# Optimization experiments

Hardware: AMD Instinct MI355X
Metric: run time of the kernel (lower is better)

The kernel has to match this reference:

```python
import jax, jax.numpy as jnp
import numpy as np

B, N = 2048, 64
D, H = 64, 256
CARD_V, UNIT_V, ENEMY_V, AT_V, SRC_V, MODE_V, TER_V, SITE_V, SKILL_V = 400, 100, 120, 50, 30, 10, 12, 25, 60
STATE_SC, CE_SC, SITE_SC, ME_SC, ACT_SC = 64, 8, 6, 8, 16
L_HAND, L_UNIT, L_CE, L_SK, L_VS, L_ME, L_TGT = 16, 8, 8, 8, 16, 16, 8
STATE_IN = STATE_SC + 6 * D + (D + CE_SC) + (D + SITE_SC) + (D + ME_SC)  # 662
ACT_IN = 7 * D + ACT_SC  # 464


def setup_inputs() -> dict:
    key = jax.random.key(0)
    ks = iter(jax.random.split(key, 64))
    nrm = lambda shape, s=1.0: jax.random.normal(next(ks), shape, jnp.float32) * s
    ri = lambda shape, hi: jax.random.randint(next(ks), shape, 0, hi, jnp.int32)
    return {
        'state_scalars': nrm((B, STATE_SC)),
        'mode_id': ri((B,), MODE_V), 'terrain_id': ri((B,), TER_V), 'site_type_id': ri((B,), SITE_V),
        'hand_ids': ri((B, L_HAND), CARD_V), 'hand_mask': ri((B, L_HAND), 2),
        'unit_ids': ri((B, L_UNIT), UNIT_V), 'unit_mask': ri((B, L_UNIT), 2),
        'combat_enemy_ids': ri((B, L_CE), ENEMY_V), 'combat_enemy_scalars': nrm((B, L_CE, CE_SC)), 'combat_enemy_mask': ri((B, L_CE), 2),
        'skill_ids': ri((B, L_SK), SKILL_V), 'skill_mask': ri((B, L_SK), 2),
        'visible_site_ids': ri((B, L_VS), SITE_V), 'visible_site_scalars': nrm((B, L_VS, SITE_SC)), 'visible_site_mask': ri((B, L_VS), 2),
        'map_enemy_ids': ri((B, L_ME), ENEMY_V), 'map_enemy_scalars': nrm((B, L_ME, ME_SC)), 'map_enemy_mask': ri((B, L_ME), 2),
        'action_ids': ri((B, N, 6), SRC_V),  # SRC_V=30 is min over the 6 id vocabs -> always in range
        'action_scalars': nrm((B, N, ACT_SC)),
        'target_enemy_ids': ri((B, N, L_TGT), ENEMY_V), 'target_mask': ri((B, N, L_TGT), 2),
        'card_emb': nrm((CARD_V, D), 0.05), 'unit_emb': nrm((UNIT_V, D), 0.05), 'enemy_emb': nrm((ENEMY_V, D), 0.05),
        'action_type_emb': nrm((AT_V, D), 0.05), 'source_emb': nrm((SRC_V, D), 0.05), 'mode_emb': nrm((MODE_V, D), 0.05),
        'terrain_emb': nrm((TER_V, D), 0.05), 'site_emb': nrm((SITE_V, D), 0.05), 'skill_emb': nrm((SKILL_V, D), 0.05),
        'map_site_emb': nrm((SITE_V, D), 0.05),
        'W_s': nrm((STATE_IN, H), 0.02), 'b_s': jnp.zeros((H,), jnp.float32),
        'W_a': nrm((ACT_IN, H), 0.02), 'b_a': jnp.zeros((H,), jnp.float32),
        'W1': nrm((2 * H, H), 0.02), 'b1': jnp.zeros((H,), jnp.float32),
        'W2': nrm((H, 1), 0.02), 'b2': jnp.zeros((1,), jnp.float32),
        'W_v': nrm((H, 1), 0.02), 'b_v': jnp.zeros((1,), jnp.float32),
    }


def masked_mean(x, mask):
    # x: [..., L, D'], mask: [..., L] (0/1). Empty list -> zeros (count clamped to 1).
    m = mask.astype(x.dtype)[..., None]
    s = jnp.sum(x * m, axis=-2)
    c = jnp.maximum(jnp.sum(m, axis=-2), 1.0)
    return s / c


def reference(state_scalars, mode_id, terrain_id, site_type_id, hand_ids, hand_mask,
              unit_ids, unit_mask, combat_enemy_ids, combat_enemy_scalars, combat_enemy_mask,
              skill_ids, skill_mask, visible_site_ids, visible_site_scalars, visible_site_mask,
              map_enemy_ids, map_enemy_scalars, map_enemy_mask, action_ids, action_scalars,
              target_enemy_ids, target_mask, card_emb, unit_emb, enemy_emb, action_type_emb,
              source_emb, mode_emb, terrain_emb, site_emb, skill_emb, map_site_emb,
              W_s, b_s, W_a, b_a, W1, b1, W2, b2, W_v, b_v):
    # ---- state encoding (batched version of encode_state) ----
    hand_pool = masked_mean(card_emb[hand_ids], hand_mask)            # [B, D]
    unit_pool = masked_mean(unit_emb[unit_ids], unit_mask)            # [B, D]
    ce = jnp.concatenate([enemy_emb[combat_enemy_ids], combat_enemy_scalars], axis=-1)
    ce_pool = masked_mean(ce, combat_enemy_mask)                      # [B, D+CE_SC]
    skill_pool = masked_mean(skill_emb[skill_ids], skill_mask)        # [B, D]
    vs = jnp.concatenate([map_site_emb[visible_site_ids], visible_site_scalars], axis=-1)
    vs_pool = masked_mean(vs, visible_site_mask)                      # [B, D+SITE_SC]
    me = jnp.concatenate([enemy_emb[map_enemy_ids], map_enemy_scalars], axis=-1)
    me_pool = masked_mean(me, map_enemy_mask)                         # [B, D+ME_SC]
    state_input = jnp.concatenate([
        state_scalars, mode_emb[mode_id], hand_pool, unit_pool,
        terrain_emb[terrain_id], site_emb[site_type_id],
        ce_pool, skill_pool, vs_pool, me_pool], axis=-1)              # [B, 662]
    state_repr = jnp.tanh(state_input @ W_s + b_s)                    # [B, H]
    # ---- action encoding (batched encode_actions) ----
    tgt_pool = masked_mean(enemy_emb[target_enemy_ids], target_mask)  # [B, N, D]
    action_input = jnp.concatenate([
        action_type_emb[action_ids[..., 0]], source_emb[action_ids[..., 1]],
        card_emb[action_ids[..., 2]], unit_emb[action_ids[..., 3]],
        enemy_emb[action_ids[..., 4]], skill_emb[action_ids[..., 5]],
        tgt_pool, action_scalars], axis=-1)                           # [B, N, 464]
    action_reprs = jnp.tanh(action_input @ W_a + b_a)                 # [B, N, H]
    # ---- scoring + value heads ----
    state_b = jnp.broadcast_to(state_repr[:, None, :], (state_repr.shape[0], action_reprs.shape[1], state_repr.shape[1]))
    combined = jnp.concatenate([state_b, action_reprs], axis=-1)      # [B, N, 2H]
    logits = (jnp.tanh(combined @ W1 + b1) @ W2 + b2)[..., 0]         # [B, N]
    value = (state_repr @ W_v + b_v)[..., 0]                          # [B]
    return logits, value
```

## Files before the change

kernel.cpp:

```cpp
#include <hip/hip_runtime.h>
#include <hip/hip_bf16.h>

#define BB 2048
#define NN 64
#define DD 64
#define HH 256
#define L_HAND 16
#define L_UNIT 8
#define L_CE 8
#define L_SK 8
#define L_VS 16
#define L_ME 16
#define L_TGT 8
#define STATE_SC 64
#define CE_SC 8
#define SITE_SC 6
#define ME_SC 8
#define ACT_SC 16
#define STATE_IN 662
#define ACT_IN 464

#define SROWS 4
#define SK 672
#define SSTRIDE 676

typedef __attribute__((ext_vector_type(8))) short short8;
typedef __attribute__((ext_vector_type(4))) float f32x4;

__device__ __forceinline__ float fast_tanh(float x) {
    float e = __expf(2.0f * x);
    return 1.0f - 2.0f / (e + 1.0f);
}
__device__ __forceinline__ short f2bs(float x) {
    __hip_bfloat16 h = __float2bfloat16(x);
    return *reinterpret_cast<short*>(&h);
}
__device__ __forceinline__ float bs2f(short u) {
    union { unsigned int i; float f; } v;
    v.i = ((unsigned int)(unsigned short)u) << 16;
    return v.f;
}

#define RO_AT    0
#define RO_SRC   50
#define RO_CARD  80
#define RO_UNIT  480
#define RO_ENEMY 580
#define RO_SKILL 700
#define EMB_ROWS 760

#define T0 (480 * 256)
#define T1 (T0 + 256 * 256)
#define T2 (T1 + EMB_ROWS * 64)
#define T3 (T2 + SK * 256)
#define T4 (T3 + 256 * 256)

__global__ __launch_bounds__(256) void pack_kernel(
    const float* __restrict__ W_a, const float* __restrict__ W1,
    const float* __restrict__ W_s,
    const float* __restrict__ at_emb, const float* __restrict__ src_emb,
    const float* __restrict__ card_emb, const float* __restrict__ unit_emb,
    const float* __restrict__ enemy_emb, const float* __restrict__ skill_emb,
    ushort* __restrict__ WaP, ushort* __restrict__ W1bP, ushort* __restrict__ emb16,
    ushort* __restrict__ WsP, ushort* __restrict__ W1aP)
{
    const int idx = blockIdx.x * 256 + threadIdx.x;
    if (idx < T0) {
        const int k = idx >> 8, n = idx & 255;
        const float v = (k < ACT_IN) ? W_a[k * HH + n] : 0.f;
        const int pi = (((k >> 5) * 16 + (n >> 4)) * 64 +
                        ((n & 15) + 16 * ((k >> 3) & 3))) * 8 + (k & 7);
        WaP[pi] = (ushort)f2bs(v);
    } else if (idx < T1) {
        const int j = idx - T0;
        const int k = j >> 8, n = j & 255;
        const float v = W1[(256 + k) * HH + n];
        const int pi = (((k >> 5) * 16 + (n >> 4)) * 64 +
                        ((n & 15) + 16 * ((k >> 3) & 3))) * 8 + (k & 7);
        W1bP[pi] = (ushort)f2bs(v);
    } else if (idx < T2) {
        const int j = idx - T1;
        const int row = j >> 6, d = j & 63;
        float v;
        if      (row < RO_SRC)   v = at_emb[row * 64 + d];
        else if (row < RO_CARD)  v = src_emb[(row - RO_SRC) * 64 + d];
        else if (row < RO_UNIT)  v = card_emb[(row - RO_CARD) * 64 + d];
        else if (row < RO_ENEMY) v = unit_emb[(row - RO_UNIT) * 64 + d];
        else if (row < RO_SKILL) v = enemy_emb[(row - RO_ENEMY) * 64 + d];
        else                     v = skill_emb[(row - RO_SKILL) * 64 + d];
        emb16[j] = (ushort)f2bs(v);
    } else if (idx < T3) {
        const int j = idx - T2;
        const int k = j >> 8, n = j & 255;
        const float v = (k < STATE_IN) ? W_s[k * HH + n] : 0.f;
        const int pi = (((k >> 5) * 16 + (n >> 4)) * 64 +
                        ((n & 15) + 16 * ((k >> 3) & 3))) * 8 + (k & 7);
        WsP[pi] = (ushort)f2bs(v);
    } else if (idx < T4) {
        const int j = idx - T3;
        const int k = j >> 8, n = j & 255;
        const float v = W1[k * HH + n];
        const int pi = (((k >> 5) * 16 + (n >> 4)) * 64 +
                        ((n & 15) + 16 * ((k >> 3) & 3))) * 8 + (k & 7);
        W1aP[pi] = (ushort)f2bs(v);
    }
}

__global__ __launch_bounds__(256) void state_mfma_kernel(
    const float* __restrict__ state_scalars,
    const int* __restrict__ mode_id, const int* __restrict__ terrain_id,
    const int* __restrict__ site_type_id,
    const int* __restrict__ hand_ids, const int* __restrict__ hand_mask,
    const int* __restrict__ unit_ids, const int* __restrict__ unit_mask,
    const int* __restrict__ ce_ids, const float* __restrict__ ce_sc, const int* __restrict__ ce_mask,
    const int* __restrict__ skill_ids, const int* __restrict__ skill_mask,
    const int* __restrict__ vs_ids, const float* __restrict__ vs_sc, const int* __restrict__ vs_mask,
    const int* __restrict__ me_ids, const float* __restrict__ me_sc, const int* __restrict__ me_mask,
    const float* __restrict__ card_emb, const float* __restrict__ unit_emb,
    const float* __restrict__ enemy_emb, const float* __restrict__ mode_emb,
    const float* __restrict__ ter_emb, const float* __restrict__ site_emb,
    const float* __restrict__ skill_emb, const float* __restrict__ msite_emb,
    const ushort* __restrict__ WsP, const float* __restrict__ b_s,
    const ushort* __restrict__ W1aP,
    const float* __restrict__ W_v, const float* __restrict__ b_v,
    float* __restrict__ s_part, float* __restrict__ out_value)
{
    __shared__ float s_in[SROWS * SSTRIDE];
    __shared__ ushort sA2[8 * 64 * 8];
    __shared__ float red[4][4];

    const int t = threadIdx.x;
    const int b0 = blockIdx.x * SROWS;
    const int w = t >> 6;
    const int lane = t & 63;

    for (int r = 0; r < SROWS; ++r) {
        const int b = b0 + r;
        for (int o = t; o < SK; o += 256) {
            float v;
            if (o >= STATE_IN) {
                v = 0.f;
            } else if (o < 64) {
                v = state_scalars[b * STATE_SC + o];
            } else if (o < 128) {
                v = mode_emb[mode_id[b] * DD + (o - 64)];
            } else if (o < 192) {
                const int d = o - 128; float s = 0.f; int c = 0;
                for (int l = 0; l < L_HAND; ++l) {
                    const int m = hand_mask[b * L_HAND + l]; c += m;
                    if (m) s += card_emb[hand_ids[b * L_HAND + l] * DD + d];
                }
                v = s / (float)(c > 1 ? c : 1);
            } else if (o < 256) {
                const int d = o - 192; float s = 0.f; int c = 0;
                for (int l = 0; l < L_UNIT; ++l) {
                    const int m = unit_mask[b * L_UNIT + l]; c += m;
                    if (m) s += unit_emb[unit_ids[b * L_UNIT + l] * DD + d];
                }
                v = s / (float)(c > 1 ? c : 1);
            } else if (o < 320) {
                v = ter_emb[terrain_id[b] * DD + (o - 256)];
            } else if (o < 384) {
                v = site_emb[site_type_id[b] * DD + (o - 320)];
            } else if (o < 456) {
                const int d = o - 384; float s = 0.f; int c = 0;
                for (int l = 0; l < L_CE; ++l) {
                    const int m = ce_mask[b * L_CE + l]; c += m;
                    if (m) s += (d < 64) ? enemy_emb[ce_ids[b * L_CE + l] * DD + d]
                                         : ce_sc[(b * L_CE + l) * CE_SC + (d - 64)];
                }
                v = s / (float)(c > 1 ? c : 1);
            } else if (o < 520) {
                const int d = o - 456; float s = 0.f; int c = 0;
                for (int l = 0; l < L_SK; ++l) {
                    const int m = skill_mask[b * L_SK + l]; c += m;
                    if (m) s += skill_emb[skill_ids[b * L_SK + l] * DD + d];
                }
                v = s / (float)(c > 1 ? c : 1);
            } else if (o < 590) {
                const int d = o - 520; float s = 0.f; int c = 0;
                for (int l = 0; l < L_VS; ++l) {
                    const int m = vs_mask[b * L_VS + l]; c += m;
                    if (m) s += (d < 64) ? msite_emb[vs_ids[b * L_VS + l] * DD + d]
                                         : vs_sc[(b * L_VS + l) * SITE_SC + (d - 64)];
                }
                v = s / (float)(c > 1 ? c : 1);
            } else {
                const int d = o - 590; float s = 0.f; int c = 0;
                for (int l = 0; l < L_ME; ++l) {
                    const int m = me_mask[b * L_ME + l]; c += m;
                    if (m) s += (d < 64) ? enemy_emb[me_ids[b * L_ME + l] * DD + d]
                                         : me_sc[(b * L_ME + l) * ME_SC + (d - 64)];
                }
                v = s / (float)(c > 1 ? c : 1);
            }
            s_in[r * SSTRIDE + o] = v;
        }
    }
    __syncthreads();

    const short8* Ws8  = (const short8*)WsP;
    const short8* W1a8 = (const short8*)W1aP;
    const f32x4 zero = {0.f, 0.f, 0.f, 0.f};
    const int m15 = lane & 15;
    const int g = lane >> 4;
    const float* arow = s_in + (m15 & 3) * SSTRIDE;

    f32x4 acc1[4];
#pragma unroll
    for (int nt = 0; nt < 4; ++nt) acc1[nt] = zero;

    for (int kt = 0; kt < 21; ++kt) {
        const int k0 = kt * 32 + 8 * g;
        const float4 v0 = *(const float4*)(arow + k0);
        const float4 v1 = *(const float4*)(arow + k0 + 4);
        short8 a;
        a[0] = f2bs(v0.x); a[1] = f2bs(v0.y); a[2] = f2bs(v0.z); a[3] = f2bs(v0.w);
        a[4] = f2bs(v1.x); a[5] = f2bs(v1.y); a[6] = f2bs(v1.z); a[7] = f2bs(v1.w);
        short8 bfr[4];
#pragma unroll
        for (int nt = 0; nt < 4; ++nt) bfr[nt] = Ws8[(kt * 16 + w * 4 + nt) * 64 + lane];
#pragma unroll
        for (int nt = 0; nt < 4; ++nt)
            acc1[nt] = __builtin_amdgcn_mfma_f32_16x16x32_bf16(a, bfr[nt], acc1[nt], 0, 0, 0);
    }

    float sr[4][4];
    float pv[4] = {0.f, 0.f, 0.f, 0.f};
#pragma unroll
    for (int nt = 0; nt < 4; ++nt) {
        const int n = w * 64 + nt * 16 + m15;
        const float bsn = b_s[n];
        const float wvn = W_v[n];
#pragma unroll
        for (int r = 0; r < 4; ++r) {
            const float sv = fast_tanh(acc1[nt][r] + bsn);
            sr[nt][r] = sv;
            pv[r] = fmaf(sv, wvn, pv[r]);
        }
    }
#pragma unroll
    for (int r = 0; r < 4; ++r) {
        float v = pv[r];
        v += __shfl_xor(v, 1);
        v += __shfl_xor(v, 2);
        v += __shfl_xor(v, 4);
        v += __shfl_xor(v, 8);
        if (lane == 0) red[w][r] = v;
    }
    if (g == 0) {
#pragma unroll
        for (int nt = 0; nt < 4; ++nt) {
            const int n = w * 64 + nt * 16 + m15;
            const int kt2 = n >> 5;
            const int lo16 = (n >> 3) & 3;
#pragma unroll
            for (int r = 0; r < 4; ++r) {
                const int pi = (kt2 * 64 + (r + 16 * lo16)) * 8 + (n & 7);
                sA2[pi] = (ushort)f2bs(sr[nt][r]);
            }
        }
    }
    __syncthreads();

    if (t < SROWS) {
        out_value[b0 + t] = red[0][t] + red[1][t] + red[2][t] + red[3][t] + b_v[0];
    }

    const short8* sA2_8 = (const short8*)sA2;
    f32x4 acc2[4];
#pragma unroll
    for (int nt = 0; nt < 4; ++nt) acc2[nt] = zero;
#pragma unroll
    for (int kt = 0; kt < 8; ++kt) {
        const short8 a2 = sA2_8[kt * 64 + lane];
        short8 bfr[4];
#pragma unroll
        for (int nt = 0; nt < 4; ++nt) bfr[nt] = W1a8[(kt * 16 + w * 4 + nt) * 64 + lane];
#pragma unroll
        for (int nt = 0; nt < 4; ++nt)
            acc2[nt] = __builtin_amdgcn_mfma_f32_16x16x32_bf16(a2, bfr[nt], acc2[nt], 0, 0, 0);
    }
    if (g == 0) {
#pragma unroll
        for (int nt = 0; nt < 4; ++nt) {
            const int n = w * 64 + nt * 16 + m15;
#pragma unroll
            for (int r = 0; r < 4; ++r)
                s_part[(b0 + r) * HH + n] = acc2[nt][r];
        }
    }
}

__global__ __launch_bounds__(512) void action_mfma_kernel(
    const int* __restrict__ action_ids, const float* __restrict__ action_scalars,
    const int* __restrict__ tgt_ids, const int* __restrict__ tgt_mask,
    const ushort* __restrict__ emb16,
    const ushort* __restrict__ WaP, const float* __restrict__ b_a,
    const ushort* __restrict__ W1bP, const float* __restrict__ b1,
    const float* __restrict__ W2, const float* __restrict__ b2,
    const float* __restrict__ s_part, float* __restrict__ out_logits)
{
    __shared__ ushort sA[15 * 4 * 64 * 8];
    __shared__ float red[8][64];
    __shared__ int s_ids[64 * 6];
    __shared__ int s_tid[64 * 8];
    __shared__ int s_tmk[64 * 8];

    const int t = threadIdx.x;
    const int b = blockIdx.x;
    const int w = t >> 6;
    const int lane = t & 63;

    for (int i = t; i < 64 * 6; i += 512) s_ids[i] = action_ids[b * (64 * 6) + i];
    for (int i = t; i < 64 * 8; i += 512) {
        s_tid[i] = tgt_ids[b * (64 * 8) + i];
        s_tmk[i] = tgt_mask[b * (64 * 8) + i];
    }
    __syncthreads();

    {
        const int m = lane;
        const int mt = m >> 4;
        const int mrow = m & 15;
        const ushort* enemy16 = emb16 + RO_ENEMY * 64;
        short8* sA8w = (short8*)sA;
        for (int kc = w; kc < 60; kc += 8) {
            const int k0 = kc << 3;
            short8 val;
            if (k0 < 384) {
                const int j = k0 >> 6;
                int roff;
                if      (j == 0) roff = RO_AT;
                else if (j == 1) roff = RO_SRC;
                else if (j == 2) roff = RO_CARD;
                else if (j == 3) roff = RO_UNIT;
                else if (j == 4) roff = RO_ENEMY;
                else             roff = RO_SKILL;
                const int id = s_ids[m * 6 + j];
                val = *(const short8*)(emb16 + (roff + id) * 64 + (k0 & 63));
            } else if (k0 < 448) {
                const int d = k0 - 384;
                float accq[8] = {0.f, 0.f, 0.f, 0.f, 0.f, 0.f, 0.f, 0.f};
                int c = 0;
#pragma unroll
                for (int l = 0; l < L_TGT; ++l) {
                    const int mk = s_tmk[m * 8 + l];
                    c += mk;
                    const float fm = (float)mk;
                    const short8 e = *(const short8*)(enemy16 + s_tid[m * 8 + l] * 64 + d);
#pragma unroll
                    for (int q = 0; q < 8; ++q) accq[q] = fmaf(fm, bs2f(e[q]), accq[q]);
                }
                const float inv = 1.0f / (float)(c > 1 ? c : 1);
#pragma unroll
                for (int q = 0; q < 8; ++q) val[q] = f2bs(accq[q] * inv);
            } else if (k0 < 464) {
                const float* sc = action_scalars + (b * NN + m) * ACT_SC + (k0 - 448);
                const float4 f0 = *(const float4*)sc;
                const float4 f1 = *(const float4*)(sc + 4);
                val[0] = f2bs(f0.x); val[1] = f2bs(f0.y); val[2] = f2bs(f0.z); val[3] = f2bs(f0.w);
                val[4] = f2bs(f1.x); val[5] = f2bs(f1.y); val[6] = f2bs(f1.z); val[7] = f2bs(f1.w);
            } else {
#pragma unroll
                for (int q = 0; q < 8; ++q) val[q] = 0;
            }
            const int kt = k0 >> 5, lo = (k0 >> 3) & 3;
            sA8w[(kt * 4 + mt) * 64 + mrow + 16 * lo] = val;
        }
    }
    __syncthreads();

    const short8* sA8  = (const short8*)sA;
    const short8* Wa8  = (const short8*)WaP;
    const short8* W1b8 = (const short8*)W1bP;
    const f32x4 zero = {0.f, 0.f, 0.f, 0.f};
    const int m15 = lane & 15;

    float ba[2];
#pragma unroll
    for (int nt = 0; nt < 2; ++nt) ba[nt] = b_a[w * 32 + nt * 16 + m15];

    f32x4 acc[4][2];
#pragma unroll
    for (int i = 0; i < 4; ++i) { acc[i][0] = zero; acc[i][1] = zero; }

    short8 bn0 = Wa8[(w * 2 + 0) * 64 + lane];
    short8 bn1 = Wa8[(w * 2 + 1) * 64 + lane];
#pragma unroll
    for (int kt = 0; kt < 15; ++kt) {
        const short8 b0 = bn0, b1 = bn1;
        if (kt < 14) {
            bn0 = Wa8[((kt + 1) * 16 + w * 2 + 0) * 64 + lane];
            bn1 = Wa8[((kt + 1) * 16 + w * 2 + 1) * 64 + lane];
        }
        short8 a[4];
#pragma unroll
        for (int mti = 0; mti < 4; ++mti) a[mti] = sA8[(kt * 4 + mti) * 64 + lane];
#pragma unroll
        for (int mti = 0; mti < 4; ++mti) {
            acc[mti][0] = __builtin_amdgcn_mfma_f32_16x16x32_bf16(a[mti], b0, acc[mti][0], 0, 0, 0);
            acc[mti][1] = __builtin_amdgcn_mfma_f32_16x16x32_bf16(a[mti], b1, acc[mti][1], 0, 0, 0);
        }
    }

    __syncthreads();

    short8 cn0 = W1b8[(w * 2 + 0) * 64 + lane];
    short8 cn1 = W1b8[(w * 2 + 1) * 64 + lane];

#pragma unroll
    for (int mti = 0; mti < 4; ++mti)
#pragma unroll
        for (int nt = 0; nt < 2; ++nt) {
            const int n = w * 32 + nt * 16 + m15;
            const int kt2 = n >> 5;
            const int lo16 = (n >> 3) & 3;
#pragma unroll
            for (int r = 0; r < 4; ++r) {
                const int mm = mti * 16 + (lane >> 4) * 4 + r;
                const float h = fast_tanh(acc[mti][nt][r] + ba[nt]);
                const int pi = ((kt2 * 4 + mti) * 64 + ((mm & 15) + 16 * lo16)) * 8 + (n & 7);
                sA[pi] = (ushort)f2bs(h);
            }
        }
    __syncthreads();

    float sp[2], w2v[2];
#pragma unroll
    for (int nt = 0; nt < 2; ++nt) {
        const int n = w * 32 + nt * 16 + m15;
        sp[nt]  = s_part[b * HH + n] + b1[n];
        w2v[nt] = W2[n];
    }

#pragma unroll
    for (int i = 0; i < 4; ++i) { acc[i][0] = zero; acc[i][1] = zero; }

#pragma unroll
    for (int kt = 0; kt < 8; ++kt) {
        const short8 b0 = cn0, b1 = cn1;
        if (kt < 7) {
            cn0 = W1b8[((kt + 1) * 16 + w * 2 + 0) * 64 + lane];
            cn1 = W1b8[((kt + 1) * 16 + w * 2 + 1) * 64 + lane];
        }
        short8 a[4];
#pragma unroll
        for (int mti = 0; mti < 4; ++mti) a[mti] = sA8[(kt * 4 + mti) * 64 + lane];
#pragma unroll
        for (int mti = 0; mti < 4; ++mti) {
            acc[mti][0] = __builtin_amdgcn_mfma_f32_16x16x32_bf16(a[mti], b0, acc[mti][0], 0, 0, 0);
            acc[mti][1] = __builtin_amdgcn_mfma_f32_16x16x32_bf16(a[mti], b1, acc[mti][1], 0, 0, 0);
        }
    }

    float part[4][4];
#pragma unroll
    for (int mti = 0; mti < 4; ++mti)
#pragma unroll
        for (int r = 0; r < 4; ++r) part[mti][r] = 0.f;

#pragma unroll
    for (int mti = 0; mti < 4; ++mti)
#pragma unroll
        for (int nt = 0; nt < 2; ++nt)
#pragma unroll
            for (int r = 0; r < 4; ++r)
                part[mti][r] += fast_tanh(acc[mti][nt][r] + sp[nt]) * w2v[nt];

#pragma unroll
    for (int mti = 0; mti < 4; ++mti)
#pragma unroll
        for (int r = 0; r < 4; ++r) {
            float v = part[mti][r];
            v += __shfl_xor(v, 1);
            v += __shfl_xor(v, 2);
            v += __shfl_xor(v, 4);
            v += __shfl_xor(v, 8);
            part[mti][r] = v;
        }
    if (m15 == 0) {
#pragma unroll
        for (int mti = 0; mti < 4; ++mti)
#pragma unroll
            for (int r = 0; r < 4; ++r) {
                const int mm = mti * 16 + (lane >> 4) * 4 + r;
                red[w][mm] = part[mti][r];
            }
    }
    __syncthreads();
    if (t < 64) {
        float s = b2[0];
#pragma unroll
        for (int wi = 0; wi < 8; ++wi) s += red[wi][t];
        out_logits[b * NN + t] = s;
    }
}

extern "C" void kernel_launch(void* const* d_in, const int* in_sizes, int n_in,
                              void* d_out, int out_size, void* d_ws, size_t ws_size,
                              hipStream_t stream) {
    const float* state_scalars = (const float*)d_in[0];
    const int*   mode_id       = (const int*)d_in[1];
    const int*   terrain_id    = (const int*)d_in[2];
    const int*   site_type_id  = (const int*)d_in[3];
    const int*   hand_ids      = (const int*)d_in[4];
    const int*   hand_mask     = (const int*)d_in[5];
    const int*   unit_ids      = (const int*)d_in[6];
    const int*   unit_mask     = (const int*)d_in[7];
    const int*   ce_ids        = (const int*)d_in[8];
    const float* ce_sc         = (const float*)d_in[9];
    const int*   ce_mask       = (const int*)d_in[10];
    const int*   skill_ids     = (const int*)d_in[11];
    const int*   skill_mask    = (const int*)d_in[12];
    const int*   vs_ids        = (const int*)d_in[13];
    const float* vs_sc         = (const float*)d_in[14];
    const int*   vs_mask       = (const int*)d_in[15];
    const int*   me_ids        = (const int*)d_in[16];
    const float* me_sc         = (const float*)d_in[17];
    const int*   me_mask       = (const int*)d_in[18];
    const int*   action_ids    = (const int*)d_in[19];
    const float* action_scalars= (const float*)d_in[20];
    const int*   tgt_ids       = (const int*)d_in[21];
    const int*   tgt_mask      = (const int*)d_in[22];
    const float* card_emb      = (const float*)d_in[23];
    const float* unit_emb      = (const float*)d_in[24];
    const float* enemy_emb     = (const float*)d_in[25];
    const float* at_emb        = (const float*)d_in[26];
    const float* src_emb       = (const float*)d_in[27];
    const float* mode_emb      = (const float*)d_in[28];
    const float* ter_emb       = (const float*)d_in[29];
    const float* site_emb      = (const float*)d_in[30];
    const float* skill_emb     = (const float*)d_in[31];
    const float* msite_emb     = (const float*)d_in[32];
    const float* W_s           = (const float*)d_in[33];
    const float* b_s           = (const float*)d_in[34];
    const float* W_a           = (const float*)d_in[35];
    const float* b_a           = (const float*)d_in[36];
    const float* W1            = (const float*)d_in[37];
    const float* b1            = (const float*)d_in[38];
    const float* W2            = (const float*)d_in[39];
    const float* b2            = (const float*)d_in[40];
    const float* W_v           = (const float*)d_in[41];
    const float* b_v           = (const float*)d_in[42];

    float* out_logits = (float*)d_out;
    float* out_value  = (float*)d_out + (size_t)BB * NN;

    char* ws = (char*)d_ws;
    float*  s_part = (float*)ws;
    ushort* WaP    = (ushort*)(ws + 2097152);
    ushort* W1bP   = (ushort*)(ws + 2342912);
    ushort* emb16  = (ushort*)(ws + 2473984);
    ushort* WsP    = (ushort*)(ws + 2571264);
    ushort* W1aP   = (ushort*)(ws + 2915328);

    pack_kernel<<<(T4 + 255) / 256, 256, 0, stream>>>(
        W_a, W1, W_s, at_emb, src_emb, card_emb, unit_emb, enemy_emb, skill_emb,
        WaP, W1bP, emb16, WsP, W1aP);

    state_mfma_kernel<<<BB / SROWS, 256, 0, stream>>>(
        state_scalars, mode_id, terrain_id, site_type_id,
        hand_ids, hand_mask, unit_ids, unit_mask,
        ce_ids, ce_sc, ce_mask, skill_ids, skill_mask,
        vs_ids, vs_sc, vs_mask, me_ids, me_sc, me_mask,
        card_emb, unit_emb, enemy_emb, mode_emb, ter_emb, site_emb,
        skill_emb, msite_emb,
        WsP, b_s, W1aP, W_v, b_v, s_part, out_value);

    action_mfma_kernel<<<BB, 512, 0, stream>>>(
        action_ids, action_scalars, tgt_ids, tgt_mask,
        emb16, WaP, b_a, W1bP, b1, W2, b2, s_part, out_logits);
}
```

Measured before the change: 132.5 us.

## Vectorize state gathers with bf16 tables and split action A-tile into halves

The state kernel's per-element gather loop becomes per-thread 8-wide chunk work. It uses vector loads and the bf16 packed embedding tables for card, unit, enemy and skill, and uses branchless masked FMAs in place of scalar fp32 reads. The action kernel builds its A operand in two halves. The shared buffer shrinks from 15 to 8 k-tiles, and the second half is rebuilt after the first half's MFMAs. This cuts LDS use, which may raise occupancy, but it adds two barriers and serializes the gather with compute. Reading bf16 embeddings in the state path also slightly changes numerics.

```diff
diff --git a/kernel.cpp b/kernel.cpp
--- a/kernel.cpp
+++ b/kernel.cpp
@@ -116,10 +116,9 @@
     const int* __restrict__ skill_ids, const int* __restrict__ skill_mask,
     const int* __restrict__ vs_ids, const float* __restrict__ vs_sc, const int* __restrict__ vs_mask,
     const int* __restrict__ me_ids, const float* __restrict__ me_sc, const int* __restrict__ me_mask,
-    const float* __restrict__ card_emb, const float* __restrict__ unit_emb,
-    const float* __restrict__ enemy_emb, const float* __restrict__ mode_emb,
-    const float* __restrict__ ter_emb, const float* __restrict__ site_emb,
-    const float* __restrict__ skill_emb, const float* __restrict__ msite_emb,
+    const float* __restrict__ mode_emb, const float* __restrict__ ter_emb,
+    const float* __restrict__ site_emb, const float* __restrict__ msite_emb,
+    const ushort* __restrict__ emb16,
     const ushort* __restrict__ WsP, const float* __restrict__ b_s,
     const ushort* __restrict__ W1aP,
     const float* __restrict__ W_v, const float* __restrict__ b_v,
@@ -133,68 +132,171 @@
     const int b0 = blockIdx.x * SROWS;
     const int w = t >> 6;
     const int lane = t & 63;
-
-    for (int r = 0; r < SROWS; ++r) {
-        const int b = b0 + r;
-        for (int o = t; o < SK; o += 256) {
-            float v;
-            if (o >= STATE_IN) {
-                v = 0.f;
-            } else if (o < 64) {
-                v = state_scalars[b * STATE_SC + o];
-            } else if (o < 128) {
-                v = mode_emb[mode_id[b] * DD + (o - 64)];
-            } else if (o < 192) {
-                const int d = o - 128; float s = 0.f; int c = 0;
-                for (int l = 0; l < L_HAND; ++l) {
-                    const int m = hand_mask[b * L_HAND + l]; c += m;
-                    if (m) s += card_emb[hand_ids[b * L_HAND + l] * DD + d];
-                }
-                v = s / (float)(c > 1 ? c : 1);
-            } else if (o < 256) {
-                const int d = o - 192; float s = 0.f; int c = 0;
-                for (int l = 0; l < L_UNIT; ++l) {
-                    const int m = unit_mask[b * L_UNIT + l]; c += m;
-                    if (m) s += unit_emb[unit_ids[b * L_UNIT + l] * DD + d];
-                }
-                v = s / (float)(c > 1 ? c : 1);
-            } else if (o < 320) {
-                v = ter_emb[terrain_id[b] * DD + (o - 256)];
-            } else if (o < 384) {
-                v = site_emb[site_type_id[b] * DD + (o - 320)];
-            } else if (o < 456) {
-                const int d = o - 384; float s = 0.f; int c = 0;
-                for (int l = 0; l < L_CE; ++l) {
-                    const int m = ce_mask[b * L_CE + l]; c += m;
-                    if (m) s += (d < 64) ? enemy_emb[ce_ids[b * L_CE + l] * DD + d]
-                                         : ce_sc[(b * L_CE + l) * CE_SC + (d - 64)];
-                }
-                v = s / (float)(c > 1 ? c : 1);
-            } else if (o < 520) {
-                const int d = o - 456; float s = 0.f; int c = 0;
-                for (int l = 0; l < L_SK; ++l) {
-                    const int m = skill_mask[b * L_SK + l]; c += m;
-                    if (m) s += skill_emb[skill_ids[b * L_SK + l] * DD + d];
-                }
-                v = s / (float)(c > 1 ? c : 1);
-            } else if (o < 590) {
-                const int d = o - 520; float s = 0.f; int c = 0;
-                for (int l = 0; l < L_VS; ++l) {
-                    const int m = vs_mask[b * L_VS + l]; c += m;
-                    if (m) s += (d < 64) ? msite_emb[vs_ids[b * L_VS + l] * DD + d]
-                                         : vs_sc[(b * L_VS + l) * SITE_SC + (d - 64)];
-                }
-                v = s / (float)(c > 1 ? c : 1);
-            } else {
-                const int d = o - 590; float s = 0.f; int c = 0;
-                for (int l = 0; l < L_ME; ++l) {
-                    const int m = me_mask[b * L_ME + l]; c += m;
-                    if (m) s += (d < 64) ? enemy_emb[me_ids[b * L_ME + l] * DD + d]
-                                         : me_sc[(b * L_ME + l) * ME_SC + (d - 64)];
-                }
-                v = s / (float)(c > 1 ? c : 1);
-            }
-            s_in[r * SSTRIDE + o] = v;
+    const ushort* card16  = emb16 + RO_CARD  * 64;
+    const ushort* unit16  = emb16 + RO_UNIT  * 64;
+    const ushort* enemy16 = emb16 + RO_ENEMY * 64;
+    const ushort* skill16 = emb16 + RO_SKILL * 64;
+
+    for (int u = t; u < SROWS * 84; u += 256) {
+        const int r  = u / 84;
+        const int un = u - r * 84;
+        const int b  = b0 + r;
+        float* dst = s_in + r * SSTRIDE;
+        if (un < 8) {
+            const int o0 = un * 8;
+            const float4 f0 = *(const float4*)(state_scalars + b * STATE_SC + o0);
+            const float4 f1 = *(const float4*)(state_scalars + b * STATE_SC + o0 + 4);
+            *(float4*)(dst + o0) = f0; *(float4*)(dst + o0 + 4) = f1;
+        } else if (un < 16) {
+            const int d0 = (un - 8) * 8;
+            const float4 f0 = *(const float4*)(mode_emb + mode_id[b] * DD + d0);
+            const float4 f1 = *(const float4*)(mode_emb + mode_id[b] * DD + d0 + 4);
+            *(float4*)(dst + 64 + d0) = f0; *(float4*)(dst + 64 + d0 + 4) = f1;
+        } else if (un < 24) {
+            const int d0 = (un - 16) * 8;
+            float acc[8] = {0,0,0,0,0,0,0,0}; int c = 0;
+#pragma unroll
+            for (int l = 0; l < L_HAND; ++l) {
+                const int mk = hand_mask[b * L_HAND + l]; c += mk;
+                const float fm = (float)mk;
+                const short8 e = *(const short8*)(card16 + hand_ids[b * L_HAND + l] * 64 + d0);
+#pragma unroll
+                for (int q = 0; q < 8; ++q) acc[q] = fmaf(fm, bs2f(e[q]), acc[q]);
+            }
+            const float inv = 1.0f / (float)(c > 1 ? c : 1);
+#pragma unroll
+            for (int q = 0; q < 8; ++q) dst[128 + d0 + q] = acc[q] * inv;
+        } else if (un < 32) {
+            const int d0 = (un - 24) * 8;
+            float acc[8] = {0,0,0,0,0,0,0,0}; int c = 0;
+#pragma unroll
+            for (int l = 0; l < L_UNIT; ++l) {
+                const int mk = unit_mask[b * L_UNIT + l]; c += mk;
+                const float fm = (float)mk;
+                const short8 e = *(const short8*)(unit16 + unit_ids[b * L_UNIT + l] * 64 + d0);
+#pragma unroll
+                for (int q = 0; q < 8; ++q) acc[q] = fmaf(fm, bs2f(e[q]), acc[q]);
+            }
+            const float inv = 1.0f / (float)(c > 1 ? c : 1);
+#pragma unroll
+            for (int q = 0; q < 8; ++q) dst[192 + d0 + q] = acc[q] * inv;
+        } else if (un < 40) {
+            const int d0 = (un - 32) * 8;
+            const float4 f0 = *(const float4*)(ter_emb + terrain_id[b] * DD + d0);
+            const float4 f1 = *(const float4*)(ter_emb + terrain_id[b] * DD + d0 + 4);
+            *(float4*)(dst + 256 + d0) = f0; *(float4*)(dst + 256 + d0 + 4) = f1;
+        } else if (un < 48) {
+            const int d0 = (un - 40) * 8;
+            const float4 f0 = *(const float4*)(site_emb + site_type_id[b] * DD + d0);
+            const float4 f1 = *(const float4*)(site_emb + site_type_id[b] * DD + d0 + 4);
+            *(float4*)(dst + 320 + d0) = f0; *(float4*)(dst + 320 + d0 + 4) = f1;
+        } else if (un < 56) {
+            const int d0 = (un - 48) * 8;
+            float acc[8] = {0,0,0,0,0,0,0,0}; int c = 0;
+#pragma unroll
+            for (int l = 0; l < L_CE; ++l) {
+                const int mk = ce_mask[b * L_CE + l]; c += mk;
+                const float fm = (float)mk;
+                const short8 e = *(const short8*)(enemy16 + ce_ids[b * L_CE + l] * 64 + d0);
+#pragma unroll
+                for (int q = 0; q < 8; ++q) acc[q] = fmaf(fm, bs2f(e[q]), acc[q]);
+            }
+            const float inv = 1.0f / (float)(c > 1 ? c : 1);
+#pragma unroll
+            for (int q = 0; q < 8; ++q) dst[384 + d0 + q] = acc[q] * inv;
+        } else if (un == 56) {
+            float acc[8] = {0,0,0,0,0,0,0,0}; int c = 0;
+#pragma unroll
+            for (int l = 0; l < L_CE; ++l) {
+                const int mk = ce_mask[b * L_CE + l]; c += mk;
+                const float fm = (float)mk;
+                const float4 f0 = *(const float4*)(ce_sc + (b * L_CE + l) * CE_SC);
+                const float4 f1 = *(const float4*)(ce_sc + (b * L_CE + l) * CE_SC + 4);
+                acc[0] = fmaf(fm, f0.x, acc[0]); acc[1] = fmaf(fm, f0.y, acc[1]);
+                acc[2] = fmaf(fm, f0.z, acc[2]); acc[3] = fmaf(fm, f0.w, acc[3]);
+                acc[4] = fmaf(fm, f1.x, acc[4]); acc[5] = fmaf(fm, f1.y, acc[5]);
+                acc[6] = fmaf(fm, f1.z, acc[6]); acc[7] = fmaf(fm, f1.w, acc[7]);
+            }
+            const float inv = 1.0f / (float)(c > 1 ? c : 1);
+#pragma unroll
+            for (int q = 0; q < 8; ++q) dst[448 + q] = acc[q] * inv;
+        } else if (un < 65) {
+            const int d0 = (un - 57) * 8;
+            float acc[8] = {0,0,0,0,0,0,0,0}; int c = 0;
+#pragma unroll
+            for (int l = 0; l < L_SK; ++l) {
+                const int mk = skill_mask[b * L_SK + l]; c += mk;
+                const float fm = (float)mk;
+                const short8 e = *(const short8*)(skill16 + skill_ids[b * L_SK + l] * 64 + d0);
+#pragma unroll
+                for (int q = 0; q < 8; ++q) acc[q] = fmaf(fm, bs2f(e[q]), acc[q]);
+            }
+            const float inv = 1.0f / (float)(c > 1 ? c : 1);
+#pragma unroll
+            for (int q = 0; q < 8; ++q) dst[456 + d0 + q] = acc[q] * inv;
+        } else if (un < 73) {
+            const int d0 = (un - 65) * 8;
+            float acc[8] = {0,0,0,0,0,0,0,0}; int c = 0;
+#pragma unroll
+            for (int l = 0; l < L_VS; ++l) {
+                const int mk = vs_mask[b * L_VS + l]; c += mk;
+                const float fm = (float)mk;
+                const float4 f0 = *(const float4*)(msite_emb + vs_ids[b * L_VS + l] * DD + d0);
+                const float4 f1 = *(const float4*)(msite_emb + vs_ids[b * L_VS + l] * DD + d0 + 4);
+                acc[0] = fmaf(fm, f0.x, acc[0]); acc[1] = fmaf(fm, f0.y, acc[1]);
+                acc[2] = fmaf(fm, f0.z, acc[2]); acc[3] = fmaf(fm, f0.w, acc[3]);
+                acc[4] = fmaf(fm, f1.x, acc[4]); acc[5] = fmaf(fm, f1.y, acc[5]);
+                acc[6] = fmaf(fm, f1.z, acc[6]); acc[7] = fmaf(fm, f1.w, acc[7]);
+            }
+            const float inv = 1.0f / (float)(c > 1 ? c : 1);
+#pragma unroll
+            for (int q = 0; q < 8; ++q) dst[520 + d0 + q] = acc[q] * inv;
+        } else if (un == 73) {
+            float acc[6] = {0,0,0,0,0,0}; int c = 0;
+#pragma unroll
+            for (int l = 0; l < L_VS; ++l) {
+                const int mk = vs_mask[b * L_VS + l]; c += mk;
+                const float fm = (float)mk;
+                const float* p = vs_sc + (b * L_VS + l) * SITE_SC;
+#pragma unroll
+                for (int q = 0; q < 6; ++q) acc[q] = fmaf(fm, p[q], acc[q]);
+            }
+            const float inv = 1.0f / (float)(c > 1 ? c : 1);
+#pragma unroll
+            for (int q = 0; q < 6; ++q) dst[584 + q] = acc[q] * inv;
+        } else if (un < 82) {
+            const int d0 = (un - 74) * 8;
+            float acc[8] = {0,0,0,0,0,0,0,0}; int c = 0;
+#pragma unroll
+            for (int l = 0; l < L_ME; ++l) {
+                const int mk = me_mask[b * L_ME + l]; c += mk;
+                const float fm = (float)mk;
+                const short8 e = *(const short8*)(enemy16 + me_ids[b * L_ME + l] * 64 + d0);
+#pragma unroll
+                for (int q = 0; q < 8; ++q) acc[q] = fmaf(fm, bs2f(e[q]), acc[q]);
+            }
+            const float inv = 1.0f / (float)(c > 1 ? c : 1);
+#pragma unroll
+            for (int q = 0; q < 8; ++q) dst[590 + d0 + q] = acc[q] * inv;
+        } else if (un == 82) {
+            float acc[8] = {0,0,0,0,0,0,0,0}; int c = 0;
+#pragma unroll
+            for (int l = 0; l < L_ME; ++l) {
+                const int mk = me_mask[b * L_ME + l]; c += mk;
+                const float fm = (float)mk;
+                const float4 f0 = *(const float4*)(me_sc + (b * L_ME + l) * ME_SC);
+                const float4 f1 = *(const float4*)(me_sc + (b * L_ME + l) * ME_SC + 4);
+                acc[0] = fmaf(fm, f0.x, acc[0]); acc[1] = fmaf(fm, f0.y, acc[1]);
+                acc[2] = fmaf(fm, f0.z, acc[2]); acc[3] = fmaf(fm, f0.w, acc[3]);
+                acc[4] = fmaf(fm, f1.x, acc[4]); acc[5] = fmaf(fm, f1.y, acc[5]);
+                acc[6] = fmaf(fm, f1.z, acc[6]); acc[7] = fmaf(fm, f1.w, acc[7]);
+            }
+            const float inv = 1.0f / (float)(c > 1 ? c : 1);
+#pragma unroll
+            for (int q = 0; q < 8; ++q) dst[654 + q] = acc[q] * inv;
+        } else {
+#pragma unroll
+            for (int q = 0; q < 10; ++q) dst[662 + q] = 0.f;
         }
     }
     __syncthreads();
@@ -290,6 +392,55 @@
                 s_part[(b0 + r) * HH + n] = acc2[nt][r];
         }
     }
+}
+
+__device__ __forceinline__ short8 build_chunk(
+    int kc, int m, int b,
+    const int* __restrict__ s_ids, const int* __restrict__ s_tid,
+    const int* __restrict__ s_tmk, const ushort* __restrict__ emb16,
+    const float* __restrict__ action_scalars)
+{
+    const int k0 = kc << 3;
+    short8 val;
+    if (k0 < 384) {
+        const int j = k0 >> 6;
+        int roff;
+        if      (j == 0) roff = RO_AT;
+        else if (j == 1) roff = RO_SRC;
+        else if (j == 2) roff = RO_CARD;
+        else if (j == 3) roff = RO_UNIT;
+        else if (j == 4) roff = RO_ENEMY;
+        else             roff = RO_SKILL;
+        const int id = s_ids[m * 6 + j];
+        val = *(const short8*)(emb16 + (roff + id) * 64 + (k0 & 63));
+    } else if (k0 < 448) {
+        const int d = k0 - 384;
+        const ushort* enemy16 = emb16 + RO_ENEMY * 64;
+        float accq[8] = {0.f, 0.f, 0.f, 0.f, 0.f, 0.f, 0.f, 0.f};
+        int c = 0;
+#pragma unroll
+        for (int l = 0; l < L_TGT; ++l) {
+            const int mk = s_tmk[m * 8 + l];
+            c += mk;
+            const float fm = (float)mk;
+            const short8 e = *(const short8*)(enemy16 + s_tid[m * 8 + l] * 64 + d);
+#pragma unroll
+            for (int q = 0; q < 8; ++q) accq[q] = fmaf(fm, bs2f(e[q]), accq[q]);
+        }
+        const float inv = 1.0f / (float)(c > 1 ? c : 1);
+#pragma unroll
+        for (int q = 0; q < 8; ++q) val[q] = f2bs(accq[q] * inv);
+    } else if (k0 < 464) {
+        const float* sc = action_scalars + (b * NN + m) * ACT_SC + (k0 - 448);
+        const float4 f0 = *(const float4*)sc;
+        const float4 f1 = *(const float4*)(sc + 4);
+        val[0] = f2bs(f0.x); val[1] = f2bs(f0.y); val[2] = f2bs(f0.z); val[3] = f2bs(f0.w);
+        val[4] = f2bs(f1.x); val[5] = f2bs(f1.y); val[6] = f2bs(f1.z); val[7] = f2bs(f1.w);
+    } else {
+#pragma unroll
+        for (int q = 0; q < 8; ++q) val[q] = 0;
+    }
+    return val;
 }
 
 __global__ __launch_bounds__(512) void action_mfma_kernel(
@@ -301,7 +452,7 @@
     const float* __restrict__ W2, const float* __restrict__ b2,
     const float* __restrict__ s_part, float* __restrict__ out_logits)
 {
-    __shared__ ushort sA[15 * 4 * 64 * 8];
+    __shared__ ushort sA[8 * 4 * 64 * 8];
     __shared__ float red[8][64];
     __shared__ int s_ids[64 * 6];
     __shared__ int s_tid[64 * 8];
@@ -319,63 +470,21 @@
     }
     __syncthreads();
 
-    {
-        const int m = lane;
-        const int mt = m >> 4;
-        const int mrow = m & 15;
-        const ushort* enemy16 = emb16 + RO_ENEMY * 64;
-        short8* sA8w = (short8*)sA;
-        for (int kc = w; kc < 60; kc += 8) {
-            const int k0 = kc << 3;
-            short8 val;
-            if (k0 < 384) {
-                const int j = k0 >> 6;
-                int roff;
-                if      (j == 0) roff = RO_AT;
-                else if (j == 1) roff = RO_SRC;
-                else if (j == 2) roff = RO_CARD;
-                else if (j == 3) roff = RO_UNIT;
-                else if (j == 4) roff = RO_ENEMY;
-                else             roff = RO_SKILL;
-                const int id = s_ids[m * 6 + j];
-                val = *(const short8*)(emb16 + (roff + id) * 64 + (k0 & 63));
-            } else if (k0 < 448) {
-                const int d = k0 - 384;
-                float accq[8] = {0.f, 0.f, 0.f, 0.f, 0.f, 0.f, 0.f, 0.f};
-                int c = 0;
-#pragma unroll
-                for (int l = 0; l < L_TGT; ++l) {
-                    const int mk = s_tmk[m * 8 + l];
-                    c += mk;
-                    const float fm = (float)mk;
-                    const short8 e = *(const short8*)(enemy16 + s_tid[m * 8 + l] * 64 + d);
-#pragma unroll
-                    for (int q = 0; q < 8; ++q) accq[q] = fmaf(fm, bs2f(e[q]), accq[q]);
-                }
-                const float inv = 1.0f / (float)(c > 1 ? c : 1);
-#pragma unroll
-                for (int q = 0; q < 8; ++q) val[q] = f2bs(accq[q] * inv);
-            } else if (k0 < 464) {
-                const float* sc = action_scalars + (b * NN + m) * ACT_SC + (k0 - 448);
-                const float4 f0 = *(const float4*)sc;
-                const float4 f1 = *(const float4*)(sc + 4);
-                val[0] = f2bs(f0.x); val[1] = f2bs(f0.y); val[2] = f2bs(f0.z); val[3] = f2bs(f0.w);
-                val[4] = f2bs(f1.x); val[5] = f2bs(f1.y); val[6] = f2bs(f1.z); val[7] = f2bs(f1.w);
-            } else {
-#pragma unroll
-                for (int q = 0; q < 8; ++q) val[q] = 0;
-            }
-            const int kt = k0 >> 5, lo = (k0 >> 3) & 3;
-            sA8w[(kt * 4 + mt) * 64 + mrow + 16 * lo] = val;
-        }
-    }
-    __syncthreads();
-
     const short8* sA8  = (const short8*)sA;
+    short8* sA8w = (short8*)sA;
     const short8* Wa8  = (const short8*)WaP;
     const short8* W1b8 = (const short8*)W1bP;
     const f32x4 zero = {0.f, 0.f, 0.f, 0.f};
     const int m15 = lane & 15;
+    const int m = lane;
+    const int mt_b = m >> 4, mrow = m & 15;
+
+    for (int kc = w; kc < 32; kc += 8) {
+        const short8 val = build_chunk(kc, m, b, s_ids, s_tid, s_tmk, emb16, action_scalars);
+        const int kt = kc >> 2, lo = kc & 3;
+        sA8w[(kt * 4 + mt_b) * 64 + mrow + 16 * lo] = val;
+    }
+    __syncthreads();
 
     float ba[2];
 #pragma unroll
@@ -388,7 +497,30 @@
     short8 bn0 = Wa8[(w * 2 + 0) * 64 + lane];
     short8 bn1 = Wa8[(w * 2 + 1) * 64 + lane];
 #pragma unroll
-    for (int kt = 0; kt < 15; ++kt) {
+    for (int kt = 0; kt < 8; ++kt) {
+        const short8 b0 = bn0, b1 = bn1;
+        bn0 = Wa8[((kt + 1) * 16 + w * 2 + 0) * 64 + lane];
+        bn1 = Wa8[((kt + 1) * 16 + w * 2 + 1) * 64 + lane];
+        short8 a[4];
+#pragma unroll
+        for (int mti = 0; mti < 4; ++mti) a[mti] = sA8[(kt * 4 + mti) * 64 + lane];
+#pragma unroll
+        for (int mti = 0; mti < 4; ++mti) {
+            acc[mti][0] = __builtin_amdgcn_mfma_f32_16x16x32_bf16(a[mti], b0, acc[mti][0], 0, 0, 0);
+            acc[mti][1] = __builtin_amdgcn_mfma_f32_16x16x32_bf16(a[mti], b1, acc[mti][1], 0, 0, 0);
+        }
+    }
+    __syncthreads();
+
+    for (int kc = 32 + w; kc < 60; kc += 8) {
+        const short8 val = build_chunk(kc, m, b, s_ids, s_tid, s_tmk, emb16, action_scalars);
+        const int ktl = (kc >> 2) - 8, lo = kc & 3;
+        sA8w[(ktl * 4 + mt_b) * 64 + mrow + 16 * lo] = val;
+    }
+    __syncthreads();
+
+#pragma unroll
+    for (int kt = 8; kt < 15; ++kt) {
         const short8 b0 = bn0, b1 = bn1;
         if (kt < 14) {
             bn0 = Wa8[((kt + 1) * 16 + w * 2 + 0) * 64 + lane];
@@ -396,14 +528,13 @@
         }
         short8 a[4];
 #pragma unroll
-        for (int mti = 0; mti < 4; ++mti) a[mti] = sA8[(kt * 4 + mti) * 64 + lane];
+        for (int mti = 0; mti < 4; ++mti) a[mti] = sA8[((kt - 8) * 4 + mti) * 64 + lane];
 #pragma unroll
         for (int mti = 0; mti < 4; ++mti) {
             acc[mti][0] = __builtin_amdgcn_mfma_f32_16x16x32_bf16(a[mti], b0, acc[mti][0], 0, 0, 0);
             acc[mti][1] = __builtin_amdgcn_mfma_f32_16x16x32_bf16(a[mti], b1, acc[mti][1], 0, 0, 0);
         }
     }
-
     __syncthreads();
 
     short8 cn0 = W1b8[(w * 2 + 0) * 64 + lane];
@@ -564,8 +695,7 @@
         hand_ids, hand_mask, unit_ids, unit_mask,
         ce_ids, ce_sc, ce_mask, skill_ids, skill_mask,
         vs_ids, vs_sc, vs_mask, me_ids, me_sc, me_mask,
-        card_emb, unit_emb, enemy_emb, mode_emb, ter_emb, site_emb,
-        skill_emb, msite_emb,
+        mode_emb, ter_emb, site_emb, msite_emb, emb16,
         WsP, b_s, W1aP, W_v, b_v, s_part, out_value);
 
     action_mfma_kernel<<<BB, 512, 0, stream>>>(
```

Result: faster. 123.7 us (-6.6%).
